# Optimization experiments

Hardware: AMD Instinct MI355X
Metric: run time of the kernel (lower is better)

## Reference

```python
import jax, jax.numpy as jnp
import numpy as np

NUM_KERNELS = 256
MAX_RECEPTIVE_FIELD = 128
B, C, T = 8, 32, 2000


def _build_kernel_bank(seed=0):
    """Sample ROCKET kernels like the torch module, then densify dilated
    kernels into a single (K, Lmax) weight matrix (zeros between taps),
    center-aligned so 'same' padding semantics are preserved."""
    rng = np.random.RandomState(seed)
    lengths, dils, raw_w, biases = [], [], [], []
    for _ in range(NUM_KERNELS):
        k = int(rng.choice([7, 9, 11]))  # _sample_kernel_length
        ub = np.log2((MAX_RECEPTIVE_FIELD - 1) / (k - 1))
        d = int(2 ** rng.uniform(0.0, ub))  # _sample_dilation
        w = rng.standard_normal(k).astype(np.float32)
        w -= w.mean()  # _sample_weights: mean-centred N(0,1)
        b = rng.uniform(-1.0, 1.0)  # _sample_bias: U(-1,1)
        lengths.append(k); dils.append(d); raw_w.append(w); biases.append(b)
    # effective (dilated) length per kernel; always odd since k odd
    eff = [(k - 1) * d + 1 for k, d in zip(lengths, dils)]
    Lmax = max(eff)  # odd
    W = np.zeros((NUM_KERNELS, Lmax), dtype=np.float32)
    for i, (k, d, w) in enumerate(zip(lengths, dils, raw_w)):
        off = (Lmax - eff[i]) // 2  # center-align (difference is even)
        W[i, off:off + eff[i]:d] = w
    return W, np.asarray(biases, dtype=np.float32)


def setup_inputs() -> dict:
    key = jax.random.key(0)
    x = jax.random.normal(key, (B, 1, C, T), dtype=jnp.float32)
    W, b = _build_kernel_bank(seed=0)
    return {"x": x, "weights": jnp.asarray(W), "bias": jnp.asarray(b)}


def reference(x, weights, bias):
    # x: (B, 1, C, T); weights: (K, Lmax) densified dilated kernels; bias: (K,)
    b, _, c, t = x.shape
    k, _ = weights.shape
    xs = x.reshape(b * c, 1, t)  # each channel-series convolved independently
    # cross-correlation (matches torch conv1d), 'SAME' pad with odd Lmax is symmetric
    y = jax.lax.conv_general_dilated(
        xs, weights[:, None, :], window_strides=(1,), padding="SAME",
        dimension_numbers=("NCH", "OIH", "NCH"))  # (B*C, K, T)
    y = y + bias[None, :, None]
    y = y.reshape(b, c, k, t)
    # PPV: heaviside with value 0 at x==0 -> strictly positive indicator
    ppv = jnp.mean(jnp.where(y > 0, 1.0, 0.0), axis=-1)  # (B, C, K)
    mx = jnp.max(y, axis=-1)                              # (B, C, K)
    # interleave [ppv_i, max_i] per kernel -> (B, C, 2K)
    feats = jnp.stack([ppv, mx], axis=-1).reshape(b, c, 2 * k)
    return feats
```

## Files before the change

kernel.cpp:

```cpp
#include <hip/hip_runtime.h>
#include <hip/hip_bf16.h>

#define T_LEN   2000
#define NKER    256
#define LPAD    128
#define NE      2128
#define THREADS 512

typedef int   v4i __attribute__((ext_vector_type(4)));
typedef float v4f __attribute__((ext_vector_type(4)));

__device__ inline v4f mfma_z(v4i a, v4i b, v4f c) {
    v4f d;
    asm volatile("v_mfma_f32_16x16x32_bf16 %0, %1, %2, %3"
                 : "=&v"(d) : "v"(a), "v"(b), "v"(c));
    return d;
}
__device__ inline void mfma_acc(v4f& acc, v4i a, v4i b) {
    asm volatile("v_mfma_f32_16x16x32_bf16 %0, %1, %2, %0"
                 : "+v"(acc) : "v"(a), "v"(b));
}
__device__ inline void mfma_acc_last(v4f& acc, v4i a, v4i b) {
    asm volatile("v_mfma_f32_16x16x32_bf16 %0, %1, %2, %0\n\ts_nop 7"
                 : "+v"(acc) : "v"(a), "v"(b));
}

__device__ inline unsigned f2bf(float f) {
    return (unsigned)__builtin_bit_cast(unsigned short, __float2bfloat16(f));
}

__global__ void rocket_prep(const float* __restrict__ W, int Lmax,
                            unsigned* __restrict__ Wbf32) {
    const int k = blockIdx.x;
    const int t = threadIdx.x;
    const int l0 = 2 * t, l1 = 2 * t + 1;
    float v0 = (l0 < Lmax) ? W[k * Lmax + l0] : 0.0f;
    float v1 = (l1 < Lmax) ? W[k * Lmax + l1] : 0.0f;
    Wbf32[k * (LPAD / 2) + t] = f2bf(v0) | (f2bf(v1) << 16);
}

__global__ __launch_bounds__(THREADS, 4) void rocket_main(
    const float* __restrict__ x, const float* __restrict__ bias,
    const unsigned short* __restrict__ Wbf, float* __restrict__ out,
    int Lmax) {

    __shared__ __align__(16) uint4 sx8[2400];
    __shared__ unsigned pc[64][4];
    __shared__ float    pm[64][4];

    const int bc  = blockIdx.x;
    const int sub = blockIdx.y;
    const int tid = threadIdx.x;
    const int c0  = (Lmax - 1) >> 1;

    {
        const int base = tid * 5;
        if (base < NE) {
            float xv[12];
            #pragma unroll
            for (int i = 0; i < 12; ++i) {
                int s = base + i - c0;
                xv[i] = (s >= 0 && s < T_LEN) ? x[bc * T_LEN + s] : 0.0f;
            }
            unsigned hb[12];
            #pragma unroll
            for (int i = 0; i < 12; ++i) hb[i] = f2bf(xv[i]);
            #pragma unroll
            for (int i = 0; i < 5; ++i) {
                int p = base + i;
                if (p < NE) {
                    uint4 v;
                    v.x = hb[i]     | (hb[i + 1] << 16);
                    v.y = hb[i + 2] | (hb[i + 3] << 16);
                    v.z = hb[i + 4] | (hb[i + 5] << 16);
                    v.w = hb[i + 6] | (hb[i + 7] << 16);
                    sx8[p + (p >> 3)] = v;
                }
            }
        }
    }

    const int lane = tid & 63;
    const int wid  = tid >> 6;
    const int kp   = wid >> 2;
    const int tq   = wid & 3;
    const int g    = lane >> 4;
    const int c    = lane & 15;

    v4i afrag[2][4];
    #pragma unroll
    for (int kt = 0; kt < 2; ++kt) {
        #pragma unroll
        for (int s = 0; s < 4; ++s) {
            const unsigned short* src =
                Wbf + ((sub * 4 + kp * 2 + kt) * 16 + c) * LPAD + s * 32 + g * 8;
            afrag[kt][s] = *reinterpret_cast<const v4i*>(src);
        }
    }

    float nb[2][4];
    #pragma unroll
    for (int kt = 0; kt < 2; ++kt) {
        float4 bv = *reinterpret_cast<const float4*>(
            bias + sub * 64 + (kp * 2 + kt) * 16 + g * 4);
        nb[kt][0] = -bv.x; nb[kt][1] = -bv.y;
        nb[kt][2] = -bv.z; nb[kt][3] = -bv.w;
    }

    __syncthreads();

    unsigned cnt[2][4] = {};
    float    mx[2][4];
    #pragma unroll
    for (int kt = 0; kt < 2; ++kt)
        #pragma unroll
        for (int r = 0; r < 4; ++r) mx[kt][r] = -__builtin_inff();

    v4f zero4 = {0.f, 0.f, 0.f, 0.f};
    asm("" : "+v"(zero4));

    const int pb = g * 8 + c;
    const unsigned voff = (unsigned)(pb + (pb >> 3)) << 4;

    auto do_tile = [&](v4i b0, v4i b1, v4i b2, v4i b3) {
        #pragma unroll
        for (int kt = 0; kt < 2; ++kt) {
            v4f acc = mfma_z(afrag[kt][0], b0, zero4);
            mfma_acc(acc, afrag[kt][1], b1);
            mfma_acc(acc, afrag[kt][2], b2);
            mfma_acc_last(acc, afrag[kt][3], b3);
            #pragma unroll
            for (int r = 0; r < 4; ++r) {
                cnt[kt][r] += (acc[r] > nb[kt][r]) ? 1u : 0u;
                mx[kt][r]  = fmaxf(mx[kt][r], acc[r]);
            }
        }
    };

    const int tstart = tq * 32;
    const int nms    = (tq == 3) ? 3 : 4;

    const char* p = (const char*)sx8 + voff + 288u * (unsigned)tstart;

    v4i w[8];
    #pragma unroll
    for (int j = 0; j < 8; ++j)
        w[j] = *reinterpret_cast<const v4i*>(p + 288 * j);

    #pragma unroll 1
    for (int ms = 0; ms < nms; ++ms) {
        #pragma unroll
        for (int m = 0; m < 4; ++m) {
            do_tile(w[(2*m + 0) & 7], w[(2*m + 2) & 7],
                    w[(2*m + 4) & 7], w[(2*m + 6) & 7]);
            do_tile(w[(2*m + 1) & 7], w[(2*m + 3) & 7],
                    w[(2*m + 5) & 7], w[(2*m + 7) & 7]);
            w[(2*m + 0) & 7] = *reinterpret_cast<const v4i*>(p + 288 * (2*m + 8));
            w[(2*m + 1) & 7] = *reinterpret_cast<const v4i*>(p + 288 * (2*m + 9));
        }
        p += 2304;
    }

    if (tq == 3) {
        #pragma unroll
        for (int tt = 0; tt < 5; ++tt) {
            v4i b0 = *reinterpret_cast<const v4i*>(p + 288 * (tt + 0));
            v4i b1 = *reinterpret_cast<const v4i*>(p + 288 * (tt + 2));
            v4i b2 = *reinterpret_cast<const v4i*>(p + 288 * (tt + 4));
            v4i b3 = *reinterpret_cast<const v4i*>(p + 288 * (tt + 6));
            do_tile(b0, b1, b2, b3);
        }
    }

    #pragma unroll
    for (int kt = 0; kt < 2; ++kt) {
        #pragma unroll
        for (int r = 0; r < 4; ++r) {
            unsigned cv = cnt[kt][r];
            cv += (unsigned)__builtin_amdgcn_update_dpp(0, (int)cv, 0x128, 0xF, 0xF, true);
            cv += (unsigned)__builtin_amdgcn_update_dpp(0, (int)cv, 0x124, 0xF, 0xF, true);
            cv += (unsigned)__builtin_amdgcn_update_dpp(0, (int)cv, 0x122, 0xF, 0xF, true);
            cv += (unsigned)__builtin_amdgcn_update_dpp(0, (int)cv, 0x121, 0xF, 0xF, true);
            float mv = mx[kt][r];
            mv = fmaxf(mv, __builtin_bit_cast(float,
                 __builtin_amdgcn_update_dpp(0, __builtin_bit_cast(int, mv), 0x128, 0xF, 0xF, true)));
            mv = fmaxf(mv, __builtin_bit_cast(float,
                 __builtin_amdgcn_update_dpp(0, __builtin_bit_cast(int, mv), 0x124, 0xF, 0xF, true)));
            mv = fmaxf(mv, __builtin_bit_cast(float,
                 __builtin_amdgcn_update_dpp(0, __builtin_bit_cast(int, mv), 0x122, 0xF, 0xF, true)));
            mv = fmaxf(mv, __builtin_bit_cast(float,
                 __builtin_amdgcn_update_dpp(0, __builtin_bit_cast(int, mv), 0x121, 0xF, 0xF, true)));
            if (c == 0) {
                const int klo = (kp * 2 + kt) * 16 + g * 4 + r;
                pc[klo][tq] = cv;
                pm[klo][tq] = mv;
            }
        }
    }
    __syncthreads();

    if (tid < 64) {
        unsigned ct = pc[tid][0] + pc[tid][1] + pc[tid][2] + pc[tid][3];
        float mv = fmaxf(fmaxf(pm[tid][0], pm[tid][1]),
                         fmaxf(pm[tid][2], pm[tid][3]));
        const int kk = sub * 64 + tid;
        out[bc * (2 * NKER) + 2 * kk]     = (float)ct * (1.0f / T_LEN);
        out[bc * (2 * NKER) + 2 * kk + 1] = mv + bias[kk];
    }
}

extern "C" void kernel_launch(void* const* d_in, const int* in_sizes, int n_in,
                              void* d_out, int out_size, void* d_ws, size_t ws_size,
                              hipStream_t stream) {
    const float* x    = (const float*)d_in[0];
    const float* W    = (const float*)d_in[1];
    const float* bias = (const float*)d_in[2];
    float*       out  = (float*)d_out;

    const int Lmax = in_sizes[1] / NKER;

    unsigned* Wbf32 = (unsigned*)d_ws;

    rocket_prep<<<dim3(NKER), dim3(64), 0, stream>>>(W, Lmax, Wbf32);
    rocket_main<<<dim3(256, 4), dim3(THREADS), 0, stream>>>(
        x, bias, (const unsigned short*)Wbf32, out, Lmax);
}
```

Baseline: 37.57 us.

## Sort kernels by effective width and skip zero K-slices in MFMA sweep

Adds a scan kernel that finds each kernel's nonzero tap extent and a rank kernel that sorts kernels by the number of 32-wide K-slices they need. The weight bank is permuted so each 32-kernel group is handled together, and the main kernel then runs only the needed 1-4 MFMAs per tile through templated sweeps. This removes MFMA work spent on zero padding for short-receptive-field kernels. In exchange it adds two small launches, permuted output indexing, and a restructured load pipeline that keeps fewer input fragments in flight.

```diff
diff --git a/kernel.cpp b/kernel.cpp
--- a/kernel.cpp
+++ b/kernel.cpp
@@ -16,6 +16,12 @@
                  : "=&v"(d) : "v"(a), "v"(b), "v"(c));
     return d;
 }
+__device__ inline v4f mfma_z_last(v4i a, v4i b, v4f c) {
+    v4f d;
+    asm volatile("v_mfma_f32_16x16x32_bf16 %0, %1, %2, %3\n\ts_nop 7"
+                 : "=&v"(d) : "v"(a), "v"(b), "v"(c));
+    return d;
+}
 __device__ inline void mfma_acc(v4f& acc, v4i a, v4i b) {
     asm volatile("v_mfma_f32_16x16x32_bf16 %0, %1, %2, %0"
                  : "+v"(acc) : "v"(a), "v"(b));
@@ -29,20 +35,107 @@
     return (unsigned)__builtin_bit_cast(unsigned short, __float2bfloat16(f));
 }
 
-__global__ void rocket_prep(const float* __restrict__ W, int Lmax,
-                            unsigned* __restrict__ Wbf32) {
+__global__ void rocket_scan(const float* __restrict__ W, int Lmax,
+                            int* __restrict__ ns_arr) {
     const int k = blockIdx.x;
     const int t = threadIdx.x;
     const int l0 = 2 * t, l1 = 2 * t + 1;
     float v0 = (l0 < Lmax) ? W[k * Lmax + l0] : 0.0f;
     float v1 = (l1 < Lmax) ? W[k * Lmax + l1] : 0.0f;
-    Wbf32[k * (LPAD / 2) + t] = f2bf(v0) | (f2bf(v1) << 16);
+    int lo = 1 << 20, hi = -1;
+    if (v0 != 0.0f) { lo = l0; hi = l0; }
+    if (v1 != 0.0f) { if (l1 < lo) lo = l1; hi = l1; }
+    #pragma unroll
+    for (int m = 32; m >= 1; m >>= 1) {
+        int ol = __shfl_xor(lo, m, 64);
+        int oh = __shfl_xor(hi, m, 64);
+        lo = ol < lo ? ol : lo;
+        hi = oh > hi ? oh : hi;
+    }
+    if (t == 0) {
+        int a = 64 - lo, b = hi - 63;
+        int m = a > b ? a : b;
+        if (m < 1) m = 1;
+        if (m > 64) m = 64;
+        ns_arr[k] = (m + 15) >> 4;
+    }
+}
+
+__global__ void rocket_rank(const int* __restrict__ ns_arr,
+                            const float* __restrict__ bias,
+                            int* __restrict__ perm, int* __restrict__ ns_s,
+                            float* __restrict__ bias_s) {
+    __shared__ int ns_sh[NKER];
+    const int k = threadIdx.x;
+    ns_sh[k] = ns_arr[k];
+    __syncthreads();
+    const int ns = ns_sh[k];
+    int pos = 0;
+    for (int j = 0; j < NKER; ++j) {
+        int nj = ns_sh[j];
+        pos += (nj < ns || (nj == ns && j < k)) ? 1 : 0;
+    }
+    perm[pos]   = k;
+    bias_s[pos] = bias[k];
+    ns_s[pos]   = ns;
+}
+
+__global__ void rocket_prep(const float* __restrict__ W, int Lmax,
+                            const int* __restrict__ perm,
+                            unsigned* __restrict__ Wbf32) {
+    const int pos = blockIdx.x;
+    const int k   = perm[pos];
+    const int t   = threadIdx.x;
+    const int l0 = 2 * t, l1 = 2 * t + 1;
+    float v0 = (l0 < Lmax) ? W[k * Lmax + l0] : 0.0f;
+    float v1 = (l1 < Lmax) ? W[k * Lmax + l1] : 0.0f;
+    Wbf32[pos * (LPAD / 2) + t] = f2bf(v0) | (f2bf(v1) << 16);
+}
+
+template<int NS>
+__device__ __attribute__((always_inline)) void sweep(
+    const char* pb, int t0, int nt,
+    const v4i (&af)[2][4], const float (&nb)[2][4],
+    unsigned (&cnt)[2][4], float (&mx)[2][4], v4f zero4)
+{
+    const char* q = pb + 288u * (unsigned)(t0 + (4 - NS));
+    v4i e[NS];
+    #pragma unroll
+    for (int i = 0; i < NS; ++i)
+        e[i] = *reinterpret_cast<const v4i*>(q + 288 * (2 * i));
+
+    #pragma unroll 1
+    for (int it = 0; it < nt; ++it) {
+        #pragma unroll
+        for (int kt = 0; kt < 2; ++kt) {
+            v4f acc;
+            if (NS == 1) {
+                acc = mfma_z_last(af[kt][0], e[0], zero4);
+            } else {
+                acc = mfma_z(af[kt][0], e[0], zero4);
+                #pragma unroll
+                for (int s = 1; s < NS - 1; ++s)
+                    mfma_acc(acc, af[kt][s], e[s]);
+                mfma_acc_last(acc, af[kt][NS - 1], e[NS - 1]);
+            }
+            #pragma unroll
+            for (int r = 0; r < 4; ++r) {
+                cnt[kt][r] += (acc[r] > nb[kt][r]) ? 1u : 0u;
+                mx[kt][r]  = fmaxf(mx[kt][r], acc[r]);
+            }
+        }
+        if (it + 1 < nt) {
+            #pragma unroll
+            for (int i = 0; i + 1 < NS; ++i) e[i] = e[i + 1];
+            e[NS - 1] = *reinterpret_cast<const v4i*>(q + 288 * (2 * NS + 2 * it));
+        }
+    }
 }
 
 __global__ __launch_bounds__(THREADS, 4) void rocket_main(
-    const float* __restrict__ x, const float* __restrict__ bias,
-    const unsigned short* __restrict__ Wbf, float* __restrict__ out,
-    int Lmax) {
+    const float* __restrict__ x, const float* __restrict__ bias_s,
+    const unsigned short* __restrict__ Wbf, const int* __restrict__ perm,
+    const int* __restrict__ ns_s, float* __restrict__ out, int Lmax) {
 
     __shared__ __align__(16) uint4 sx8[2400];
     __shared__ unsigned pc[64][4];
@@ -87,22 +180,31 @@
     const int g    = lane >> 4;
     const int c    = lane & 15;
 
+    const int tile0 = sub * 4 + kp * 2;
+    const int tile1 = tile0 + 1;
+    int ns = __builtin_amdgcn_readfirstlane(ns_s[tile1 * 16 + 15]);
+    ns = ns < 1 ? 1 : (ns > 4 ? 4 : ns);
+
     v4i afrag[2][4];
+    const int l0 = 16 * (4 - ns);
     #pragma unroll
     for (int kt = 0; kt < 2; ++kt) {
+        const int tld = (kt == 0) ? tile0 : tile1;
         #pragma unroll
         for (int s = 0; s < 4; ++s) {
-            const unsigned short* src =
-                Wbf + ((sub * 4 + kp * 2 + kt) * 16 + c) * LPAD + s * 32 + g * 8;
-            afrag[kt][s] = *reinterpret_cast<const v4i*>(src);
+            if (s < ns) {
+                const unsigned short* src =
+                    Wbf + (tld * 16 + c) * LPAD + l0 + s * 32 + g * 8;
+                afrag[kt][s] = *reinterpret_cast<const v4i*>(src);
+            }
         }
     }
 
     float nb[2][4];
     #pragma unroll
     for (int kt = 0; kt < 2; ++kt) {
-        float4 bv = *reinterpret_cast<const float4*>(
-            bias + sub * 64 + (kp * 2 + kt) * 16 + g * 4);
+        const int tld = (kt == 0) ? tile0 : tile1;
+        float4 bv = *reinterpret_cast<const float4*>(bias_s + tld * 16 + g * 4);
         nb[kt][0] = -bv.x; nb[kt][1] = -bv.y;
         nb[kt][2] = -bv.z; nb[kt][3] = -bv.w;
     }
@@ -121,55 +223,29 @@
 
     const int pb = g * 8 + c;
     const unsigned voff = (unsigned)(pb + (pb >> 3)) << 4;
-
-    auto do_tile = [&](v4i b0, v4i b1, v4i b2, v4i b3) {
-        #pragma unroll
-        for (int kt = 0; kt < 2; ++kt) {
-            v4f acc = mfma_z(afrag[kt][0], b0, zero4);
-            mfma_acc(acc, afrag[kt][1], b1);
-            mfma_acc(acc, afrag[kt][2], b2);
-            mfma_acc_last(acc, afrag[kt][3], b3);
-            #pragma unroll
-            for (int r = 0; r < 4; ++r) {
-                cnt[kt][r] += (acc[r] > nb[kt][r]) ? 1u : 0u;
-                mx[kt][r]  = fmaxf(mx[kt][r], acc[r]);
-            }
-        }
-    };
+    const char* sxb = (const char*)sx8 + voff;
 
     const int tstart = tq * 32;
-    const int nms    = (tq == 3) ? 3 : 4;
-
-    const char* p = (const char*)sx8 + voff + 288u * (unsigned)tstart;
-
-    v4i w[8];
-    #pragma unroll
-    for (int j = 0; j < 8; ++j)
-        w[j] = *reinterpret_cast<const v4i*>(p + 288 * j);
-
-    #pragma unroll 1
-    for (int ms = 0; ms < nms; ++ms) {
-        #pragma unroll
-        for (int m = 0; m < 4; ++m) {
-            do_tile(w[(2*m + 0) & 7], w[(2*m + 2) & 7],
-                    w[(2*m + 4) & 7], w[(2*m + 6) & 7]);
-            do_tile(w[(2*m + 1) & 7], w[(2*m + 3) & 7],
-                    w[(2*m + 5) & 7], w[(2*m + 7) & 7]);
-            w[(2*m + 0) & 7] = *reinterpret_cast<const v4i*>(p + 288 * (2*m + 8));
-            w[(2*m + 1) & 7] = *reinterpret_cast<const v4i*>(p + 288 * (2*m + 9));
-        }
-        p += 2304;
-    }
-
-    if (tq == 3) {
-        #pragma unroll
-        for (int tt = 0; tt < 5; ++tt) {
-            v4i b0 = *reinterpret_cast<const v4i*>(p + 288 * (tt + 0));
-            v4i b1 = *reinterpret_cast<const v4i*>(p + 288 * (tt + 2));
-            v4i b2 = *reinterpret_cast<const v4i*>(p + 288 * (tt + 4));
-            v4i b3 = *reinterpret_cast<const v4i*>(p + 288 * (tt + 6));
-            do_tile(b0, b1, b2, b3);
-        }
+    const int nt_e   = (tq == 3) ? 15 : 16;
+    const int nt_o   = (tq == 3) ? 14 : 16;
+
+    switch (ns) {
+    case 1:
+        sweep<1>(sxb, tstart,     nt_e, afrag, nb, cnt, mx, zero4);
+        sweep<1>(sxb, tstart + 1, nt_o, afrag, nb, cnt, mx, zero4);
+        break;
+    case 2:
+        sweep<2>(sxb, tstart,     nt_e, afrag, nb, cnt, mx, zero4);
+        sweep<2>(sxb, tstart + 1, nt_o, afrag, nb, cnt, mx, zero4);
+        break;
+    case 3:
+        sweep<3>(sxb, tstart,     nt_e, afrag, nb, cnt, mx, zero4);
+        sweep<3>(sxb, tstart + 1, nt_o, afrag, nb, cnt, mx, zero4);
+        break;
+    default:
+        sweep<4>(sxb, tstart,     nt_e, afrag, nb, cnt, mx, zero4);
+        sweep<4>(sxb, tstart + 1, nt_o, afrag, nb, cnt, mx, zero4);
+        break;
     }
 
     #pragma unroll
@@ -203,9 +279,10 @@
         unsigned ct = pc[tid][0] + pc[tid][1] + pc[tid][2] + pc[tid][3];
         float mv = fmaxf(fmaxf(pm[tid][0], pm[tid][1]),
                          fmaxf(pm[tid][2], pm[tid][3]));
-        const int kk = sub * 64 + tid;
+        const int pos = sub * 64 + tid;
+        const int kk  = perm[pos];
         out[bc * (2 * NKER) + 2 * kk]     = (float)ct * (1.0f / T_LEN);
-        out[bc * (2 * NKER) + 2 * kk + 1] = mv + bias[kk];
+        out[bc * (2 * NKER) + 2 * kk + 1] = mv + bias_s[pos];
     }
 }
 
@@ -219,9 +296,16 @@
 
     const int Lmax = in_sizes[1] / NKER;
 
-    unsigned* Wbf32 = (unsigned*)d_ws;
-
-    rocket_prep<<<dim3(NKER), dim3(64), 0, stream>>>(W, Lmax, Wbf32);
+    unsigned* Wbf32  = (unsigned*)d_ws;
+    int*      perm   = (int*)((char*)d_ws + 65536);
+    float*    bias_s = (float*)((char*)d_ws + 66560);
+    int*      ns_arr = (int*)((char*)d_ws + 67584);
+    int*      ns_s   = (int*)((char*)d_ws + 68608);
+
+    rocket_scan<<<dim3(NKER), dim3(64), 0, stream>>>(W, Lmax, ns_arr);
+    rocket_rank<<<dim3(1), dim3(NKER), 0, stream>>>(ns_arr, bias,
+                                                    perm, ns_s, bias_s);
+    rocket_prep<<<dim3(NKER), dim3(64), 0, stream>>>(W, Lmax, perm, Wbf32);
     rocket_main<<<dim3(256, 4), dim3(THREADS), 0, stream>>>(
-        x, bias, (const unsigned short*)Wbf32, out, Lmax);
-}
+        x, bias_s, (const unsigned short*)Wbf32, perm, ns_s, out, Lmax);
+}
```

Result: slower. 53.69 us (+42.9%).

## Split time axis across blocks with partial reduction finalized in separate kernel

Applied to the files above, without the earlier changes.

Reworks the grid from (series, kernel-quarter) blocks of 512 threads into (series, kernel-half, time-chunk) blocks of 256 threads. Each block stages only a 256-sample window of the bf16 input in shared memory and writes per-chunk count/max partials to workspace. A new finalize kernel sums and maxes the eight partials per kernel. This gives many more, smaller blocks for occupancy and less LDS per block, at the cost of an extra launch, redundant halo staging, and partial traffic through global memory.

```diff
diff --git a/kernel.cpp b/kernel.cpp
--- a/kernel.cpp
+++ b/kernel.cpp
@@ -4,8 +4,7 @@
 #define T_LEN   2000
 #define NKER    256
 #define LPAD    128
-#define NE      2128
-#define THREADS 512
+#define NSTG    408
 
 typedef int   v4i __attribute__((ext_vector_type(4)));
 typedef float v4f __attribute__((ext_vector_type(4)));
@@ -39,61 +38,75 @@
     Wbf32[k * (LPAD / 2) + t] = f2bf(v0) | (f2bf(v1) << 16);
 }
 
-__global__ __launch_bounds__(THREADS, 4) void rocket_main(
+#define DO_KT4(kt, T)                                                        \
+    {                                                                        \
+        v4f acc = mfma_z(afrag[kt][0], w[(T + 0) & 7], zero4);               \
+        mfma_acc(acc, afrag[kt][1], w[(T + 2) & 7]);                         \
+        mfma_acc(acc, afrag[kt][2], w[(T + 4) & 7]);                         \
+        mfma_acc_last(acc, afrag[kt][3], w[(T + 6) & 7]);                    \
+        _Pragma("unroll")                                                    \
+        for (int r = 0; r < 4; ++r) {                                        \
+            cnt[kt][r] += (acc[r] > nb[kt][r]) ? 1u : 0u;                    \
+            mx[kt][r]  = fmaxf(mx[kt][r], acc[r]);                           \
+        }                                                                    \
+    }
+
+__global__ __launch_bounds__(256, 4) void rocket_main(
     const float* __restrict__ x, const float* __restrict__ bias,
-    const unsigned short* __restrict__ Wbf, float* __restrict__ out,
+    const unsigned short* __restrict__ Wbf, float2* __restrict__ part,
     int Lmax) {
 
-    __shared__ __align__(16) uint4 sx8[2400];
-    __shared__ unsigned pc[64][4];
-    __shared__ float    pm[64][4];
+    __shared__ __align__(16) uint4 sx8[464];
 
     const int bc  = blockIdx.x;
-    const int sub = blockIdx.y;
+    const int kh  = blockIdx.y;
+    const int tc  = blockIdx.z;
     const int tid = threadIdx.x;
     const int c0  = (Lmax - 1) >> 1;
 
     {
-        const int base = tid * 5;
-        if (base < NE) {
-            float xv[12];
-            #pragma unroll
-            for (int i = 0; i < 12; ++i) {
-                int s = base + i - c0;
+        const int base = tid * 2;
+        if (base < NSTG) {
+            const int q0 = tc * 256 + base;
+            float xv[9];
+            #pragma unroll
+            for (int i = 0; i < 9; ++i) {
+                int s = q0 + i - c0;
                 xv[i] = (s >= 0 && s < T_LEN) ? x[bc * T_LEN + s] : 0.0f;
             }
-            unsigned hb[12];
-            #pragma unroll
-            for (int i = 0; i < 12; ++i) hb[i] = f2bf(xv[i]);
-            #pragma unroll
-            for (int i = 0; i < 5; ++i) {
+            unsigned hb[9];
+            #pragma unroll
+            for (int i = 0; i < 9; ++i) hb[i] = f2bf(xv[i]);
+            #pragma unroll
+            for (int i = 0; i < 2; ++i) {
                 int p = base + i;
-                if (p < NE) {
-                    uint4 v;
-                    v.x = hb[i]     | (hb[i + 1] << 16);
-                    v.y = hb[i + 2] | (hb[i + 3] << 16);
-                    v.z = hb[i + 4] | (hb[i + 5] << 16);
-                    v.w = hb[i + 6] | (hb[i + 7] << 16);
-                    sx8[p + (p >> 3)] = v;
-                }
-            }
-        }
-    }
+                uint4 v;
+                v.x = hb[i]     | (hb[i + 1] << 16);
+                v.y = hb[i + 2] | (hb[i + 3] << 16);
+                v.z = hb[i + 4] | (hb[i + 5] << 16);
+                v.w = hb[i + 6] | (hb[i + 7] << 16);
+                sx8[p + (p >> 3)] = v;
+            }
+        }
+    }
+    __syncthreads();
 
     const int lane = tid & 63;
-    const int wid  = tid >> 6;
-    const int kp   = wid >> 2;
-    const int tq   = wid & 3;
+    const int kp   = tid >> 6;
     const int g    = lane >> 4;
     const int c    = lane & 15;
 
+    const int gt0 = kh * 8 + kp * 2;
+    const int gt1 = gt0 + 1;
+
     v4i afrag[2][4];
     #pragma unroll
     for (int kt = 0; kt < 2; ++kt) {
+        const int tld = (kt == 0) ? gt0 : gt1;
         #pragma unroll
         for (int s = 0; s < 4; ++s) {
             const unsigned short* src =
-                Wbf + ((sub * 4 + kp * 2 + kt) * 16 + c) * LPAD + s * 32 + g * 8;
+                Wbf + (tld * 16 + c) * LPAD + s * 32 + g * 8;
             afrag[kt][s] = *reinterpret_cast<const v4i*>(src);
         }
     }
@@ -101,13 +114,11 @@
     float nb[2][4];
     #pragma unroll
     for (int kt = 0; kt < 2; ++kt) {
-        float4 bv = *reinterpret_cast<const float4*>(
-            bias + sub * 64 + (kp * 2 + kt) * 16 + g * 4);
+        const int tld = (kt == 0) ? gt0 : gt1;
+        float4 bv = *reinterpret_cast<const float4*>(bias + tld * 16 + g * 4);
         nb[kt][0] = -bv.x; nb[kt][1] = -bv.y;
         nb[kt][2] = -bv.z; nb[kt][3] = -bv.w;
     }
-
-    __syncthreads();
 
     unsigned cnt[2][4] = {};
     float    mx[2][4];
@@ -121,26 +132,10 @@
 
     const int pb = g * 8 + c;
     const unsigned voff = (unsigned)(pb + (pb >> 3)) << 4;
-
-    auto do_tile = [&](v4i b0, v4i b1, v4i b2, v4i b3) {
-        #pragma unroll
-        for (int kt = 0; kt < 2; ++kt) {
-            v4f acc = mfma_z(afrag[kt][0], b0, zero4);
-            mfma_acc(acc, afrag[kt][1], b1);
-            mfma_acc(acc, afrag[kt][2], b2);
-            mfma_acc_last(acc, afrag[kt][3], b3);
-            #pragma unroll
-            for (int r = 0; r < 4; ++r) {
-                cnt[kt][r] += (acc[r] > nb[kt][r]) ? 1u : 0u;
-                mx[kt][r]  = fmaxf(mx[kt][r], acc[r]);
-            }
-        }
-    };
-
-    const int tstart = tq * 32;
-    const int nms    = (tq == 3) ? 3 : 4;
-
-    const char* p = (const char*)sx8 + voff + 288u * (unsigned)tstart;
+    const char* p = (const char*)sx8 + voff;
+
+    const bool full = (tc < 7);
+    const int  nms  = full ? 2 : 1;
 
     v4i w[8];
     #pragma unroll
@@ -149,26 +144,44 @@
 
     #pragma unroll 1
     for (int ms = 0; ms < nms; ++ms) {
-        #pragma unroll
-        for (int m = 0; m < 4; ++m) {
-            do_tile(w[(2*m + 0) & 7], w[(2*m + 2) & 7],
-                    w[(2*m + 4) & 7], w[(2*m + 6) & 7]);
-            do_tile(w[(2*m + 1) & 7], w[(2*m + 3) & 7],
-                    w[(2*m + 5) & 7], w[(2*m + 7) & 7]);
-            w[(2*m + 0) & 7] = *reinterpret_cast<const v4i*>(p + 288 * (2*m + 8));
-            w[(2*m + 1) & 7] = *reinterpret_cast<const v4i*>(p + 288 * (2*m + 9));
-        }
+        DO_KT4(0, 0) DO_KT4(1, 0)
+        DO_KT4(0, 1) DO_KT4(1, 1)
+        w[0] = *reinterpret_cast<const v4i*>(p + 288 * 8);
+        w[1] = *reinterpret_cast<const v4i*>(p + 288 * 9);
+        DO_KT4(0, 2) DO_KT4(1, 2)
+        DO_KT4(0, 3) DO_KT4(1, 3)
+        w[2] = *reinterpret_cast<const v4i*>(p + 288 * 10);
+        w[3] = *reinterpret_cast<const v4i*>(p + 288 * 11);
+        DO_KT4(0, 4) DO_KT4(1, 4)
+        DO_KT4(0, 5) DO_KT4(1, 5)
+        w[4] = *reinterpret_cast<const v4i*>(p + 288 * 12);
+        w[5] = *reinterpret_cast<const v4i*>(p + 288 * 13);
+        DO_KT4(0, 6) DO_KT4(1, 6)
+        DO_KT4(0, 7) DO_KT4(1, 7)
+        w[6] = *reinterpret_cast<const v4i*>(p + 288 * 14);
+        w[7] = *reinterpret_cast<const v4i*>(p + 288 * 15);
         p += 2304;
     }
 
-    if (tq == 3) {
-        #pragma unroll
+    if (!full) {
+        #pragma unroll 1
         for (int tt = 0; tt < 5; ++tt) {
             v4i b0 = *reinterpret_cast<const v4i*>(p + 288 * (tt + 0));
             v4i b1 = *reinterpret_cast<const v4i*>(p + 288 * (tt + 2));
             v4i b2 = *reinterpret_cast<const v4i*>(p + 288 * (tt + 4));
             v4i b3 = *reinterpret_cast<const v4i*>(p + 288 * (tt + 6));
-            do_tile(b0, b1, b2, b3);
+            #pragma unroll
+            for (int kt = 0; kt < 2; ++kt) {
+                v4f acc = mfma_z(afrag[kt][0], b0, zero4);
+                mfma_acc(acc, afrag[kt][1], b1);
+                mfma_acc(acc, afrag[kt][2], b2);
+                mfma_acc_last(acc, afrag[kt][3], b3);
+                #pragma unroll
+                for (int r = 0; r < 4; ++r) {
+                    cnt[kt][r] += (acc[r] > nb[kt][r]) ? 1u : 0u;
+                    mx[kt][r]  = fmaxf(mx[kt][r], acc[r]);
+                }
+            }
         }
     }
 
@@ -191,22 +204,28 @@
             mv = fmaxf(mv, __builtin_bit_cast(float,
                  __builtin_amdgcn_update_dpp(0, __builtin_bit_cast(int, mv), 0x121, 0xF, 0xF, true)));
             if (c == 0) {
-                const int klo = (kp * 2 + kt) * 16 + g * 4 + r;
-                pc[klo][tq] = cv;
-                pm[klo][tq] = mv;
-            }
-        }
-    }
-    __syncthreads();
-
-    if (tid < 64) {
-        unsigned ct = pc[tid][0] + pc[tid][1] + pc[tid][2] + pc[tid][3];
-        float mv = fmaxf(fmaxf(pm[tid][0], pm[tid][1]),
-                         fmaxf(pm[tid][2], pm[tid][3]));
-        const int kk = sub * 64 + tid;
-        out[bc * (2 * NKER) + 2 * kk]     = (float)ct * (1.0f / T_LEN);
-        out[bc * (2 * NKER) + 2 * kk + 1] = mv + bias[kk];
-    }
+                const int krow = ((kh * 8 + kp * 2 + kt) * 16) + g * 4 + r;
+                part[(bc * 8 + tc) * NKER + krow] =
+                    make_float2((float)cv, mv);
+            }
+        }
+    }
+}
+
+__global__ void rocket_fin(const float2* __restrict__ part,
+                           const float* __restrict__ bias,
+                           float* __restrict__ out) {
+    const int bc = blockIdx.x;
+    const int k  = threadIdx.x;
+    float cnt = 0.0f, mx = -__builtin_inff();
+    #pragma unroll
+    for (int tc = 0; tc < 8; ++tc) {
+        float2 v = part[(bc * 8 + tc) * NKER + k];
+        cnt += v.x;
+        mx = fmaxf(mx, v.y);
+    }
+    out[bc * (2 * NKER) + 2 * k]     = cnt * (1.0f / T_LEN);
+    out[bc * (2 * NKER) + 2 * k + 1] = mx + bias[k];
 }
 
 extern "C" void kernel_launch(void* const* d_in, const int* in_sizes, int n_in,
@@ -220,8 +239,10 @@
     const int Lmax = in_sizes[1] / NKER;
 
     unsigned* Wbf32 = (unsigned*)d_ws;
+    float2*   part  = (float2*)((char*)d_ws + 65536);
 
     rocket_prep<<<dim3(NKER), dim3(64), 0, stream>>>(W, Lmax, Wbf32);
-    rocket_main<<<dim3(256, 4), dim3(THREADS), 0, stream>>>(
-        x, bias, (const unsigned short*)Wbf32, out, Lmax);
-}
+    rocket_main<<<dim3(256, 2, 8), dim3(256), 0, stream>>>(
+        x, bias, (const unsigned short*)Wbf32, part, Lmax);
+    rocket_fin<<<dim3(256), dim3(NKER), 0, stream>>>(part, bias, out);
+}
```

New measurement: 44.42 us. +18.2%, slower.
